# Kernel tuning notes

Hardware: AMD Instinct MI355X
Metric: run time of the kernel (lower is better)

The kernel has to match this reference:

```python
import jax, jax.numpy as jnp
import numpy as np

B, S, H = 4, 8192, 1024


def setup_inputs() -> dict:
    key = jax.random.key(0)
    kq, kk, kv, k1, k2, k3, k4 = jax.random.split(key, 7)
    residual_init_factor = 1.0
    return {
        "q": jax.random.normal(kq, (B, S, H), dtype=jnp.float32),
        "k": jax.random.normal(kk, (B, S, H), dtype=jnp.float32),
        "v": jax.random.normal(kv, (B, S, H), dtype=jnp.float32),
        "w_q": 0.01 * jax.random.normal(k1, (H, H), dtype=jnp.float32),
        "w_k": 0.01 * jax.random.normal(k2, (H, H), dtype=jnp.float32),
        "w_v": 0.01 * jax.random.normal(k3, (H, H), dtype=jnp.float32),
        "w_p": 0.01 * residual_init_factor * jax.random.normal(k4, (H, H), dtype=jnp.float32),
    }


def reference(q, k, v, w_q, w_k, w_v, w_p):
    # Projections: [B,S,H] @ [H,H]
    emb_q = jnp.einsum("bsh,hd->bsd", q, w_q)
    emb_k = jnp.einsum("bsh,hd->bsd", k, w_k)
    emb_v = jnp.einsum("bsh,hd->bsd", v, w_v)
    # AFT-simple: per-channel exponential-weighted causal prefix average
    k_exp = jnp.exp(emb_k)
    k_exp_prefix = jnp.cumsum(k_exp, axis=1)
    k_exp_v_prefix = jnp.cumsum(k_exp * emb_v, axis=1)
    y = jax.nn.sigmoid(emb_q) * (k_exp_v_prefix / k_exp_prefix)
    return jnp.einsum("bsh,hd->bsd", y, w_p)
```

## Files before the change

kernel.cpp:

```cpp
#include <hip/hip_runtime.h>
#include <hip/hip_bf16.h>
#include <cstdint>

#define AS_GLOBAL __attribute__((address_space(1)))
#define AS_LDS    __attribute__((address_space(3)))

typedef __attribute__((ext_vector_type(8))) short bf16x8;
typedef __attribute__((ext_vector_type(8))) unsigned short u16x8;
typedef __attribute__((ext_vector_type(4))) float f32x4;

static __device__ __forceinline__ ushort f2bf(float x) {
    union { float f; uint32_t u; } c;
    c.f = x;
    uint32_t u = c.u;
    u += 0x7fffu + ((u >> 16) & 1u);
    return (ushort)(u >> 16);
}
static __device__ __forceinline__ float bf2f(ushort u) {
    union { uint32_t i; float f; } c;
    c.i = ((uint32_t)u) << 16;
    return c.f;
}

static __device__ __forceinline__ void gload_lds16(const void* g, void* l) {
    __builtin_amdgcn_global_load_lds(
        (const AS_GLOBAL uint32_t*)(uintptr_t)g,
        (AS_LDS uint32_t*)(uint32_t)(uintptr_t)l,
        16, 0, 0);
}

__global__ __launch_bounds__(256)
void cvt_f32_bf16(const float4* __restrict__ in, u16x8* __restrict__ out, int n8) {
    int i = blockIdx.x * 256 + threadIdx.x;
    int stride = gridDim.x * 256;
    for (; i < n8; i += stride) {
        float4 a = in[i * 2], b = in[i * 2 + 1];
        u16x8 o;
        o[0] = f2bf(a.x); o[1] = f2bf(a.y); o[2] = f2bf(a.z); o[3] = f2bf(a.w);
        o[4] = f2bf(b.x); o[5] = f2bf(b.y); o[6] = f2bf(b.z); o[7] = f2bf(b.w);
        out[i] = o;
    }
}

__global__ __launch_bounds__(256)
void transpose4_to_bf16(const float* __restrict__ w0, const float* __restrict__ w1,
                        const float* __restrict__ w2, const float* __restrict__ w3,
                        ushort* __restrict__ t0, ushort* __restrict__ t1,
                        ushort* __restrict__ t2, ushort* __restrict__ t3) {
    const int K = 1024, N = 1024;
    __shared__ float tile[32][33];
    const float* w; ushort* wt;
    switch (blockIdx.z) {
        case 0: w = w0; wt = t0; break;
        case 1: w = w1; wt = t1; break;
        case 2: w = w2; wt = t2; break;
        default: w = w3; wt = t3; break;
    }
    int bn = blockIdx.x * 32;
    int bk = blockIdx.y * 32;
    int tx = threadIdx.x & 31, ty = threadIdx.x >> 5;
    #pragma unroll
    for (int i = 0; i < 32; i += 8)
        tile[ty + i][tx] = w[(size_t)(bk + ty + i) * N + bn + tx];
    __syncthreads();
    #pragma unroll
    for (int i = 0; i < 32; i += 8)
        wt[(size_t)(bn + ty + i) * K + bk + tx] = f2bf(tile[tx][ty + i]);
}

template<int EPI, int OUT_BF>
__global__ __launch_bounds__(256, 2)
void gemm256x128(const ushort* __restrict__ A, const ushort* __restrict__ Bt,
                 void* __restrict__ Cv) {
    constexpr int K = 1024, N = 1024;
    __shared__ alignas(16) ushort sA[3 * 8192];
    __shared__ alignas(16) ushort sB[3 * 4096];
    const int tid  = threadIdx.x;
    const int wid  = tid >> 6;
    const int lane = tid & 63;
    const int wr = wid >> 1, wc = wid & 1;
    const int lr = lane & 15;
    const int kb = lane >> 4;
    const int xs = (lr >> 1) & 3;

    const int wg = blockIdx.x;
    const int xcd = wg & 7, local = wg >> 3;
    const int bm = xcd * 16 + (local >> 3);
    const int bn = local & 7;
    const int m0 = bm * 256, n0 = bn * 128;

    f32x4 acc[8][4] = {};

    auto stage = [&](int tile, int buf) {
        const int kt0 = tile * 32;
        ushort* dA = &sA[buf * 8192];
        ushort* dB = &sB[buf * 4096];
        #pragma unroll
        for (int j = 0; j < 4; j++) {
            int c = j * 256 + tid;
            int r = c >> 2, p = c & 3;
            int s = p ^ ((r >> 1) & 3);
            gload_lds16(A + (size_t)(m0 + r) * K + kt0 + s * 8, dA + c * 8);
        }
        #pragma unroll
        for (int j = 0; j < 2; j++) {
            int c = j * 256 + tid;
            int r = c >> 2, p = c & 3;
            int s = p ^ ((r >> 1) & 3);
            gload_lds16(Bt + (size_t)(n0 + r) * K + kt0 + s * 8, dB + c * 8);
        }
    };
    auto compute = [&](int buf) {
        const ushort* pA = &sA[buf * 8192];
        const ushort* pB = &sB[buf * 4096];
        bf16x8 af[8], bv[4];
        #pragma unroll
        for (int m = 0; m < 8; m++)
            af[m] = *(const bf16x8*)&pA[(wr * 128 + m * 16 + lr) * 32 + (kb ^ xs) * 8];
        #pragma unroll
        for (int n = 0; n < 4; n++)
            bv[n] = *(const bf16x8*)&pB[(wc * 64 + n * 16 + lr) * 32 + (kb ^ xs) * 8];
        #pragma unroll
        for (int m = 0; m < 8; m++)
            #pragma unroll
            for (int n = 0; n < 4; n++)
                acc[m][n] = __builtin_amdgcn_mfma_f32_16x16x32_bf16(af[m], bv[n], acc[m][n], 0, 0, 0);
    };

    stage(0, 0);
    stage(1, 1);
    asm volatile("s_waitcnt vmcnt(6)" ::: "memory");
    __builtin_amdgcn_s_barrier();
    asm volatile("" ::: "memory");

    for (int t = 0; t < 32; t++) {
        if (t < 30) stage(t + 2, (t + 2) % 3);
        compute(t % 3);
        if (t < 30)       asm volatile("s_waitcnt vmcnt(6)" ::: "memory");
        else if (t == 30) asm volatile("s_waitcnt vmcnt(0)" ::: "memory");
        asm volatile("s_waitcnt lgkmcnt(0)" ::: "memory");
        __builtin_amdgcn_s_barrier();
        asm volatile("" ::: "memory");
    }

    float*  Cf = (float*)Cv;
    ushort* Cb = (ushort*)Cv;
    #pragma unroll
    for (int m = 0; m < 8; m++) {
        #pragma unroll
        for (int n = 0; n < 4; n++) {
            #pragma unroll
            for (int r = 0; r < 4; r++) {
                int row = m0 + wr * 128 + m * 16 + (lane >> 4) * 4 + r;
                int col = n0 + wc * 64 + n * 16 + (lane & 15);
                float v = acc[m][n][r];
                if (EPI == 1) v = 1.0f / (1.0f + __expf(-v));
                else if (EPI == 2) v = __expf(v);
                size_t idx = (size_t)row * N + col;
                if (OUT_BF) Cb[idx] = f2bf(v);
                else        Cf[idx] = v;
            }
        }
    }
}

__global__ __launch_bounds__(256)
void scan_partials(const ushort* __restrict__ ke, const ushort* __restrict__ ev,
                   float* __restrict__ pke, float* __restrict__ pkv) {
    const int H = 1024, S = 8192, CHUNK = 32, BH = 4096;
    int c  = blockIdx.x * 2 + (threadIdx.x >> 7);
    int h0 = (threadIdx.x & 127) * 8;
    int b  = blockIdx.y;
    size_t base = ((size_t)b * S + (size_t)c * CHUNK) * H + h0;
    float se[8] = {}, sv[8] = {};
    for (int s = 0; s < CHUNK; s++) {
        u16x8 e8 = *(const u16x8*)(ke + base + (size_t)s * H);
        u16x8 v8 = *(const u16x8*)(ev + base + (size_t)s * H);
        #pragma unroll
        for (int i = 0; i < 8; i++) {
            float e = bf2f(e8[i]);
            se[i] += e;
            sv[i] += e * bf2f(v8[i]);
        }
    }
    size_t p = (size_t)c * BH + b * H + h0;
    *(float4*)(pke + p)     = make_float4(se[0], se[1], se[2], se[3]);
    *(float4*)(pke + p + 4) = make_float4(se[4], se[5], se[6], se[7]);
    *(float4*)(pkv + p)     = make_float4(sv[0], sv[1], sv[2], sv[3]);
    *(float4*)(pkv + p + 4) = make_float4(sv[4], sv[5], sv[6], sv[7]);
}

__global__ __launch_bounds__(256)
void scan_offsets(float* __restrict__ pke, float* __restrict__ pkv, int nch, int BH) {
    int i = blockIdx.x * blockDim.x + threadIdx.x;
    if (i >= BH) return;
    float rke = 0.f, rkv = 0.f;
    #pragma unroll 8
    for (int c = 0; c < nch; c++) {
        size_t idx = (size_t)c * BH + i;
        float a = pke[idx], b = pkv[idx];
        pke[idx] = rke; pkv[idx] = rkv;
        rke += a; rkv += b;
    }
}

__global__ __launch_bounds__(256)
void scan_final(const ushort* __restrict__ ke, const ushort* __restrict__ ev,
                const ushort* __restrict__ sq,
                const float* __restrict__ pke, const float* __restrict__ pkv,
                ushort* __restrict__ ybf) {
    const int H = 1024, S = 8192, CHUNK = 32, BH = 4096;
    int c  = blockIdx.x * 2 + (threadIdx.x >> 7);
    int h0 = (threadIdx.x & 127) * 8;
    int b  = blockIdx.y;
    size_t p = (size_t)c * BH + b * H + h0;
    float rke[8], rkv[8];
    *(float4*)(rke)     = *(const float4*)(pke + p);
    *(float4*)(rke + 4) = *(const float4*)(pke + p + 4);
    *(float4*)(rkv)     = *(const float4*)(pkv + p);
    *(float4*)(rkv + 4) = *(const float4*)(pkv + p + 4);
    size_t base = ((size_t)b * S + (size_t)c * CHUNK) * H + h0;
    for (int s = 0; s < CHUNK; s++) {
        size_t idx = base + (size_t)s * H;
        u16x8 e8 = *(const u16x8*)(ke + idx);
        u16x8 v8 = *(const u16x8*)(ev + idx);
        u16x8 q8 = *(const u16x8*)(sq + idx);
        u16x8 o;
        #pragma unroll
        for (int i = 0; i < 8; i++) {
            float e = bf2f(e8[i]);
            rke[i] += e;
            rkv[i] += e * bf2f(v8[i]);
            o[i] = f2bf(bf2f(q8[i]) * (rkv[i] / rke[i]));
        }
        *(u16x8*)(ybf + idx) = o;
    }
}

extern "C" void kernel_launch(void* const* d_in, const int* in_sizes, int n_in,
                              void* d_out, int out_size, void* d_ws, size_t ws_size,
                              hipStream_t stream) {
    const float* q   = (const float*)d_in[0];
    const float* k   = (const float*)d_in[1];
    const float* v   = (const float*)d_in[2];
    const float* w_q = (const float*)d_in[3];
    const float* w_k = (const float*)d_in[4];
    const float* w_v = (const float*)d_in[5];
    const float* w_p = (const float*)d_in[6];
    float* out = (float*)d_out;

    const int B = 4, S = 8192, H = 1024;
    const int M = B * S;
    const size_t MH = (size_t)M * H;
    const int NCH = 256;
    const int BH = B * H;

    char* ws = (char*)d_ws;
    size_t off = 0;
    auto alloc = [&](size_t bytes) -> char* {
        char* p = ws + off;
        off += (bytes + 255) & ~(size_t)255;
        return p;
    };
    ushort* abuf = (ushort*)alloc(MH * 2);
    ushort* wqt  = (ushort*)alloc((size_t)H * H * 2);
    ushort* wkt  = (ushort*)alloc((size_t)H * H * 2);
    ushort* wvt  = (ushort*)alloc((size_t)H * H * 2);
    ushort* wpt  = (ushort*)alloc((size_t)H * H * 2);
    ushort* sqb  = (ushort*)alloc(MH * 2);
    ushort* keb  = (ushort*)alloc(MH * 2);
    ushort* evb  = (ushort*)alloc(MH * 2);
    float*  pke  = (float*)alloc((size_t)NCH * BH * 4);
    float*  pkv  = (float*)alloc((size_t)NCH * BH * 4);

    const int ngg = (M / 256) * (H / 128);
    dim3 tg(H / 32, H / 32, 4);
    dim3 gs(NCH / 2, B);
    const int n8 = (int)(MH / 8);

    transpose4_to_bf16<<<tg, 256, 0, stream>>>(w_q, w_k, w_v, w_p, wqt, wkt, wvt, wpt);

    cvt_f32_bf16<<<2048, 256, 0, stream>>>((const float4*)q, (u16x8*)abuf, n8);
    gemm256x128<1, 1><<<ngg, 256, 0, stream>>>(abuf, wqt, sqb);
    cvt_f32_bf16<<<2048, 256, 0, stream>>>((const float4*)k, (u16x8*)abuf, n8);
    gemm256x128<2, 1><<<ngg, 256, 0, stream>>>(abuf, wkt, keb);
    cvt_f32_bf16<<<2048, 256, 0, stream>>>((const float4*)v, (u16x8*)abuf, n8);
    gemm256x128<0, 1><<<ngg, 256, 0, stream>>>(abuf, wvt, evb);

    scan_partials<<<gs, 256, 0, stream>>>(keb, evb, pke, pkv);
    scan_offsets<<<BH / 256, 256, 0, stream>>>(pke, pkv, NCH, BH);
    scan_final<<<gs, 256, 0, stream>>>(keb, evb, sqb, pke, pkv, abuf);

    gemm256x128<0, 0><<<ngg, 256, 0, stream>>>(abuf, wpt, out);
}
```

Baseline: 524.1 us.

## Restructure GEMM to 8 waves with 64-wide K tiles and split-phase pipelining

The 256x128 GEMM now runs with 512 threads (8 waves, each owning a 64x64 output), uses a K tile of 64 with an 8-way XOR swizzle, and splits each iteration into two phases. In each phase the LDS reads and half of the next stage's global-to-LDS loads are interleaved with MFMA bursts, separated by barriers and raised with s_setprio. The aim is better overlap of memory traffic with matrix math and more waves to hide latency. In exchange it adds more barriers per iteration, and LDS grows to about 144KB per block, which may limit occupancy to one block per CU despite launch_bounds(512,2).

```diff
diff --git a/kernel.cpp b/kernel.cpp
--- a/kernel.cpp
+++ b/kernel.cpp
@@ -69,19 +69,19 @@
 }
 
 template<int EPI, int OUT_BF>
-__global__ __launch_bounds__(256, 2)
-void gemm256x128(const ushort* __restrict__ A, const ushort* __restrict__ Bt,
-                 void* __restrict__ Cv) {
+__global__ __launch_bounds__(512, 2)
+void gemm8p(const ushort* __restrict__ A, const ushort* __restrict__ Bt,
+            void* __restrict__ Cv) {
     constexpr int K = 1024, N = 1024;
-    __shared__ alignas(16) ushort sA[3 * 8192];
-    __shared__ alignas(16) ushort sB[3 * 4096];
+    __shared__ alignas(16) ushort sA[3][256 * 64];
+    __shared__ alignas(16) ushort sB[3][128 * 64];
     const int tid  = threadIdx.x;
     const int wid  = tid >> 6;
     const int lane = tid & 63;
     const int wr = wid >> 1, wc = wid & 1;
     const int lr = lane & 15;
     const int kb = lane >> 4;
-    const int xs = (lr >> 1) & 3;
+    const int x7 = lr & 7;
 
     const int wg = blockIdx.x;
     const int xcd = wg & 7, local = wg >> 3;
@@ -89,56 +89,88 @@
     const int bn = local & 7;
     const int m0 = bm * 256, n0 = bn * 128;
 
-    f32x4 acc[8][4] = {};
-
-    auto stage = [&](int tile, int buf) {
-        const int kt0 = tile * 32;
-        ushort* dA = &sA[buf * 8192];
-        ushort* dB = &sB[buf * 4096];
-        #pragma unroll
-        for (int j = 0; j < 4; j++) {
-            int c = j * 256 + tid;
-            int r = c >> 2, p = c & 3;
-            int s = p ^ ((r >> 1) & 3);
-            gload_lds16(A + (size_t)(m0 + r) * K + kt0 + s * 8, dA + c * 8);
+    f32x4 acc[4][4] = {};
+    bf16x8 af[4][2];
+    bf16x8 bv[2][2];
+
+    auto stageA2 = [&](int tile, int buf, int j0) {
+        const int kt0 = tile * 64;
+        #pragma unroll
+        for (int j = 0; j < 2; j++) {
+            int c = (j0 + j) * 512 + tid;
+            int r = c >> 3, p = c & 7;
+            int s = p ^ (r & 7);
+            gload_lds16(A + (size_t)(m0 + r) * K + kt0 + s * 8, &sA[buf][c * 8]);
         }
-        #pragma unroll
-        for (int j = 0; j < 2; j++) {
-            int c = j * 256 + tid;
-            int r = c >> 2, p = c & 3;
-            int s = p ^ ((r >> 1) & 3);
-            gload_lds16(Bt + (size_t)(n0 + r) * K + kt0 + s * 8, dB + c * 8);
-        }
-    };
-    auto compute = [&](int buf) {
-        const ushort* pA = &sA[buf * 8192];
-        const ushort* pB = &sB[buf * 4096];
-        bf16x8 af[8], bv[4];
-        #pragma unroll
-        for (int m = 0; m < 8; m++)
-            af[m] = *(const bf16x8*)&pA[(wr * 128 + m * 16 + lr) * 32 + (kb ^ xs) * 8];
-        #pragma unroll
-        for (int n = 0; n < 4; n++)
-            bv[n] = *(const bf16x8*)&pB[(wc * 64 + n * 16 + lr) * 32 + (kb ^ xs) * 8];
-        #pragma unroll
-        for (int m = 0; m < 8; m++)
+    };
+    auto stageB1 = [&](int tile, int buf, int j) {
+        const int kt0 = tile * 64;
+        int c = j * 512 + tid;
+        int r = c >> 3, p = c & 7;
+        int s = p ^ (r & 7);
+        gload_lds16(Bt + (size_t)(n0 + r) * K + kt0 + s * 8, &sB[buf][c * 8]);
+    };
+    auto readA = [&](int buf) {
+        #pragma unroll
+        for (int m = 0; m < 4; m++)
             #pragma unroll
-            for (int n = 0; n < 4; n++)
-                acc[m][n] = __builtin_amdgcn_mfma_f32_16x16x32_bf16(af[m], bv[n], acc[m][n], 0, 0, 0);
-    };
-
-    stage(0, 0);
-    stage(1, 1);
+            for (int kh = 0; kh < 2; kh++)
+                af[m][kh] = *(const bf16x8*)&sA[buf][(wr * 64 + m * 16 + lr) * 64
+                                                    + ((kh * 4 + kb) ^ x7) * 8];
+    };
+    auto readB = [&](int buf, int nq) {
+        #pragma unroll
+        for (int n = 0; n < 2; n++)
+            #pragma unroll
+            for (int kh = 0; kh < 2; kh++)
+                bv[n][kh] = *(const bf16x8*)&sB[buf][(wc * 64 + nq * 32 + n * 16 + lr) * 64
+                                                    + ((kh * 4 + kb) ^ x7) * 8];
+    };
+    auto mfma16 = [&](int nq) {
+        #pragma unroll
+        for (int m = 0; m < 4; m++)
+            #pragma unroll
+            for (int n = 0; n < 2; n++) {
+                acc[m][nq * 2 + n] = __builtin_amdgcn_mfma_f32_16x16x32_bf16(
+                    af[m][0], bv[n][0], acc[m][nq * 2 + n], 0, 0, 0);
+                acc[m][nq * 2 + n] = __builtin_amdgcn_mfma_f32_16x16x32_bf16(
+                    af[m][1], bv[n][1], acc[m][nq * 2 + n], 0, 0, 0);
+            }
+    };
+
+    stageA2(0, 0, 0); stageA2(0, 0, 2); stageB1(0, 0, 0); stageB1(0, 0, 1);
+    stageA2(1, 1, 0); stageA2(1, 1, 2); stageB1(1, 1, 0); stageB1(1, 1, 1);
     asm volatile("s_waitcnt vmcnt(6)" ::: "memory");
     __builtin_amdgcn_s_barrier();
     asm volatile("" ::: "memory");
 
-    for (int t = 0; t < 32; t++) {
-        if (t < 30) stage(t + 2, (t + 2) % 3);
-        compute(t % 3);
-        if (t < 30)       asm volatile("s_waitcnt vmcnt(6)" ::: "memory");
-        else if (t == 30) asm volatile("s_waitcnt vmcnt(0)" ::: "memory");
+    for (int t = 0; t < 16; t++) {
+        const int b  = t % 3;
+        const int b2 = (t + 2) % 3;
+        const bool st = (t < 14);
+        readA(b);
+        readB(b, 0);
+        if (st) { stageA2(t + 2, b2, 0); stageB1(t + 2, b2, 0); }
+        asm volatile("" ::: "memory");
+        __builtin_amdgcn_s_barrier();
         asm volatile("s_waitcnt lgkmcnt(0)" ::: "memory");
+        __builtin_amdgcn_s_setprio(1);
+        mfma16(0);
+        __builtin_amdgcn_s_setprio(0);
+        asm volatile("" ::: "memory");
+        __builtin_amdgcn_s_barrier();
+        asm volatile("" ::: "memory");
+        readB(b, 1);
+        if (st) { stageA2(t + 2, b2, 2); stageB1(t + 2, b2, 1); }
+        asm volatile("" ::: "memory");
+        __builtin_amdgcn_s_barrier();
+        asm volatile("s_waitcnt lgkmcnt(0)" ::: "memory");
+        __builtin_amdgcn_s_setprio(1);
+        mfma16(1);
+        __builtin_amdgcn_s_setprio(0);
+        if (t < 14)       asm volatile("s_waitcnt vmcnt(6)" ::: "memory");
+        else if (t == 14) asm volatile("s_waitcnt vmcnt(0)" ::: "memory");
+        asm volatile("" ::: "memory");
         __builtin_amdgcn_s_barrier();
         asm volatile("" ::: "memory");
     }
@@ -146,12 +178,12 @@
     float*  Cf = (float*)Cv;
     ushort* Cb = (ushort*)Cv;
     #pragma unroll
-    for (int m = 0; m < 8; m++) {
+    for (int m = 0; m < 4; m++) {
         #pragma unroll
         for (int n = 0; n < 4; n++) {
             #pragma unroll
             for (int r = 0; r < 4; r++) {
-                int row = m0 + wr * 128 + m * 16 + (lane >> 4) * 4 + r;
+                int row = m0 + wr * 64 + m * 16 + (lane >> 4) * 4 + r;
                 int col = n0 + wc * 64 + n * 16 + (lane & 15);
                 float v = acc[m][n][r];
                 if (EPI == 1) v = 1.0f / (1.0f + __expf(-v));
@@ -281,15 +313,15 @@
     transpose4_to_bf16<<<tg, 256, 0, stream>>>(w_q, w_k, w_v, w_p, wqt, wkt, wvt, wpt);
 
     cvt_f32_bf16<<<2048, 256, 0, stream>>>((const float4*)q, (u16x8*)abuf, n8);
-    gemm256x128<1, 1><<<ngg, 256, 0, stream>>>(abuf, wqt, sqb);
+    gemm8p<1, 1><<<ngg, 512, 0, stream>>>(abuf, wqt, sqb);
     cvt_f32_bf16<<<2048, 256, 0, stream>>>((const float4*)k, (u16x8*)abuf, n8);
-    gemm256x128<2, 1><<<ngg, 256, 0, stream>>>(abuf, wkt, keb);
+    gemm8p<2, 1><<<ngg, 512, 0, stream>>>(abuf, wkt, keb);
     cvt_f32_bf16<<<2048, 256, 0, stream>>>((const float4*)v, (u16x8*)abuf, n8);
-    gemm256x128<0, 1><<<ngg, 256, 0, stream>>>(abuf, wvt, evb);
+    gemm8p<0, 1><<<ngg, 512, 0, stream>>>(abuf, wvt, evb);
 
     scan_partials<<<gs, 256, 0, stream>>>(keb, evb, pke, pkv);
     scan_offsets<<<BH / 256, 256, 0, stream>>>(pke, pkv, NCH, BH);
     scan_final<<<gs, 256, 0, stream>>>(keb, evb, sqb, pke, pkv, abuf);
 
-    gemm256x128<0, 0><<<ngg, 256, 0, stream>>>(abuf, wpt, out);
-}
+    gemm8p<0, 0><<<ngg, 512, 0, stream>>>(abuf, wpt, out);
+}
```

Measured after the change: 553.8 us. 1.06x slower.
